# Optimization experiments

Measured on AMD Instinct MI355X. Metric: run time of the kernel, lower is better.

The kernel has to match this reference:

```python
import jax, jax.numpy as jnp
import numpy as np

B, D, C = 2048, 512, 50000
MARGIN = 0.3
SCALE = 30.0
EPS = 1e-12


def setup_inputs() -> dict:
    key = jax.random.key(0)
    k1, k2, k3 = jax.random.split(key, 3)
    embeddings = jax.random.normal(k1, (B, D), dtype=jnp.float32)
    labels = jax.random.randint(k2, (B,), 0, C, dtype=jnp.int64)
    # Xavier-uniform init for weight (num_classes, in_features)
    limit = float(np.sqrt(6.0 / (C + D)))
    weight = jax.random.uniform(k3, (C, D), dtype=jnp.float32, minval=-limit, maxval=limit)
    return {"embeddings": embeddings, "labels": labels, "weight": weight}


def _l2_normalize(x, axis):
    # Matches torch F.normalize(p=2, eps=1e-12): x / max(||x||, eps)
    norm = jnp.sqrt(jnp.sum(x * x, axis=axis, keepdims=True))
    return x / jnp.maximum(norm, EPS)


def reference(embeddings, labels, weight):
    emb_n = _l2_normalize(embeddings, axis=1)            # (B, D)
    w_n = _l2_normalize(weight, axis=1)                  # (C, D)
    cos = jnp.einsum("bd,cd->bc", emb_n, w_n)            # (B, C)
    # margin subtract at label index (avoid dense one-hot materialization)
    rows = jnp.arange(cos.shape[0])
    phi = cos.at[rows, labels].add(-MARGIN)
    logits = phi * SCALE
    # cross-entropy with mean reduction
    logp = jax.nn.log_softmax(logits, axis=-1)
    nll = -jnp.take_along_axis(logp, labels[:, None], axis=-1)[:, 0]
    return jnp.mean(nll)
```

## Files before the change

kernel.cpp:

```cpp
#include <hip/hip_runtime.h>
#include <hip/hip_bf16.h>
#include <math.h>
#include <stdint.h>


#define B_ROWS    2048
#define D_DIM     512
#define C_CLASSES 50000
#define C_PAD     50048
#define NCHUNK    391
#define CPX       49
#define ARC_MARGIN 0.3f
#define ARC_SCALE  30.0f
#define ARC_EPS    1e-12f
#define K_LOG2E_S  43.2808512f

#define OFF_WQ    0u
#define OFF_EMBQ  25624576u
#define OFF_WINV  26673152u
#define OFF_EINV  26873152u
#define OFF_PART  26881344u

typedef __attribute__((ext_vector_type(8))) int   i32x8;
typedef __attribute__((ext_vector_type(4))) int   i32x4;
typedef __attribute__((ext_vector_type(4))) float f32x4;

typedef __attribute__((address_space(1))) const unsigned int g_u32;
typedef __attribute__((address_space(3))) unsigned int       l_u32;

__device__ __forceinline__ void gload_lds16(const void* g, void* l) {
    g_u32* gp = (g_u32*)(uintptr_t)g;
    l_u32* lp = (l_u32*)(uintptr_t)l;
    __builtin_amdgcn_global_load_lds(gp, lp, 16, 0, 0);
}

__global__ __launch_bounds__(256) void k_prep(const float* __restrict__ emb,
                                              const float* __restrict__ weight,
                                              uint8_t* __restrict__ embq,
                                              uint8_t* __restrict__ wq,
                                              float* __restrict__ einv,
                                              float* __restrict__ winv,
                                              float* __restrict__ out) {
    if (blockIdx.x == 0 && threadIdx.x == 0) out[0] = 0.f;
    int gw   = (blockIdx.x * blockDim.x + threadIdx.x) >> 6;
    int lane = threadIdx.x & 63;
    const float* src;
    uint8_t* dst;
    float* invout;
    if (gw < C_PAD) {
        if (gw >= C_CLASSES) {
            *(int2*)(wq + (size_t)gw * D_DIM + lane * 8) = make_int2(0, 0);
            return;
        }
        src = weight + (size_t)gw * D_DIM;
        dst = wq + (size_t)gw * D_DIM;
        invout = winv + gw;
    } else {
        int row = gw - C_PAD;
        src = emb + (size_t)row * D_DIM;
        dst = embq + (size_t)row * D_DIM;
        invout = einv + row;
    }
    const float4* r4 = (const float4*)src;
    float4 v0 = r4[lane * 2];
    float4 v1 = r4[lane * 2 + 1];
    float s = v0.x*v0.x + v0.y*v0.y + v0.z*v0.z + v0.w*v0.w
            + v1.x*v1.x + v1.y*v1.y + v1.z*v1.z + v1.w*v1.w;
    #pragma unroll
    for (int off = 32; off; off >>= 1) s += __shfl_xor(s, off);
    float r = 1.0f / fmaxf(sqrtf(s), ARC_EPS);
    if (lane == 0) *invout = r;
    int p0 = __builtin_amdgcn_cvt_pk_fp8_f32(v0.x * r, v0.y * r, 0, false);
    p0     = __builtin_amdgcn_cvt_pk_fp8_f32(v0.z * r, v0.w * r, p0, true);
    int p1 = __builtin_amdgcn_cvt_pk_fp8_f32(v1.x * r, v1.y * r, 0, false);
    p1     = __builtin_amdgcn_cvt_pk_fp8_f32(v1.z * r, v1.w * r, p1, true);
    *(int2*)(dst + lane * 8) = make_int2(p0, p1);
}

struct TrueT  { static constexpr bool value = true;  };
struct FalseT { static constexpr bool value = false; };

__global__ __launch_bounds__(256) void k_gemm(const uint8_t* __restrict__ embq,
                                              const uint8_t* __restrict__ wq,
                                              float* __restrict__ partials) {
    __shared__ __align__(16) uint8_t A_s[128 * 128];
    __shared__ __align__(16) uint8_t B_s[128 * 128];
    __shared__ float Red[128][2];

    const int tid    = threadIdx.x;
    const int w      = tid >> 6;
    const int lane   = tid & 63;
    const int lanelo = lane & 15;
    const int quad   = lane >> 4;
    const int wrow0  = (w >> 1) * 64;
    const int wcol0  = (w & 1) * 64;

    const int id    = blockIdx.x;
    const int xcd   = id & 7;
    const int s     = id >> 3;
    const int rb_   = s & 15;
    const int chunk = xcd * CPX + (s >> 4);
    if (chunk >= NCHUNK) return;
    const int b0 = rb_ * 128;
    const int n0 = chunk * 128;

    const uint8_t* Abase = embq + (size_t)b0 * D_DIM;
    const uint8_t* Bbase = wq   + (size_t)n0 * D_DIM;

    f32x4 acc[4][4];
    #pragma unroll
    for (int i = 0; i < 4; ++i)
        #pragma unroll
        for (int j = 0; j < 4; ++j)
            acc[i][j] = (f32x4){0.f, 0.f, 0.f, 0.f};

    const int srow = lane & 15;
    const int skc  = lane >> 4;

    auto stage = [&](int kt) {
        const int k0 = kt * 128;
        #pragma unroll
        for (int t = 0; t < 2; ++t) {
            const int rb = w * 2 + t;
            #pragma unroll
            for (int h = 0; h < 2; ++h) {
                const int kc = h * 4 + skc;
                gload_lds16(Abase + (size_t)(rb * 16 + srow) * D_DIM + k0 + kc * 16,
                            &A_s[rb * 2048 + h * 1024]);
                gload_lds16(Bbase + (size_t)(rb * 16 + srow) * D_DIM + k0 + kc * 16,
                            &B_s[rb * 2048 + h * 1024]);
            }
        }
    };

    stage(0);
    #pragma unroll
    for (int kt = 0; kt < 4; ++kt) {
        __syncthreads();

        i32x8 af[4], bfr[4];
        #pragma unroll
        for (int i = 0; i < 4; ++i) {
            const int rb = (w >> 1) * 4 + i;
            i32x4 lo = *(const i32x4*)&A_s[rb * 2048 + quad * 512 + lanelo * 16];
            i32x4 hi = *(const i32x4*)&A_s[rb * 2048 + quad * 512 + 256 + lanelo * 16];
            af[i] = (i32x8){lo[0], lo[1], lo[2], lo[3], hi[0], hi[1], hi[2], hi[3]};
        }
        #pragma unroll
        for (int j = 0; j < 4; ++j) {
            const int rb = (w & 1) * 4 + j;
            i32x4 lo = *(const i32x4*)&B_s[rb * 2048 + quad * 512 + lanelo * 16];
            i32x4 hi = *(const i32x4*)&B_s[rb * 2048 + quad * 512 + 256 + lanelo * 16];
            bfr[j] = (i32x8){lo[0], lo[1], lo[2], lo[3], hi[0], hi[1], hi[2], hi[3]};
        }
        __syncthreads();

        if (kt < 3) stage(kt + 1);

        #pragma unroll
        for (int i = 0; i < 4; ++i)
            #pragma unroll
            for (int j = 0; j < 4; ++j)
                acc[i][j] = __builtin_amdgcn_mfma_scale_f32_16x16x128_f8f6f4(
                    af[i], bfr[j], acc[i][j],
                    0, 0,
                    0, 127,
                    0, 127);
    }

    auto epi = [&](auto maskTag) {
        constexpr bool MASK = decltype(maskTag)::value;
        #pragma unroll
        for (int i = 0; i < 4; ++i) {
            #pragma unroll
            for (int reg = 0; reg < 4; ++reg) {
                float s4 = 0.f;
                #pragma unroll
                for (int j = 0; j < 4; ++j) {
                    float t = __builtin_amdgcn_exp2f(
                        fmaf(acc[i][j][reg], K_LOG2E_S, -K_LOG2E_S));
                    if (MASK) {
                        int c = n0 + wcol0 + j * 16 + lanelo;
                        if (c >= C_CLASSES) t = 0.f;
                    }
                    s4 += t;
                }
                #pragma unroll
                for (int off = 1; off < 16; off <<= 1)
                    s4 += __shfl_xor(s4, off);
                if (lanelo == 0)
                    Red[wrow0 + i * 16 + quad * 4 + reg][w & 1] = s4;
            }
        }
    };
    if (chunk == NCHUNK - 1) epi(TrueT{}); else epi(FalseT{});
    __syncthreads();

    if (tid < 128)
        partials[(size_t)(b0 + tid) * NCHUNK + chunk] = Red[tid][0] + Red[tid][1];
}

__global__ __launch_bounds__(256) void k_fin(const float* __restrict__ emb,
                                             const float* __restrict__ weight,
                                             const float* __restrict__ einv,
                                             const float* __restrict__ winv,
                                             const int* __restrict__ labels,
                                             const float* __restrict__ partials,
                                             float* __restrict__ out) {
    __shared__ float sm[4];
    int widx = threadIdx.x >> 6;
    int b    = blockIdx.x * 4 + widx;
    int lane = threadIdx.x & 63;
    int label = labels[b];

    const float4* e  = (const float4*)(emb + (size_t)b * D_DIM);
    const float4* wt = (const float4*)(weight + (size_t)label * D_DIM);
    float4 e0 = e[lane],  e1 = e[lane + 64];
    float4 w0 = wt[lane], w1 = wt[lane + 64];
    float dot = e0.x*w0.x + e0.y*w0.y + e0.z*w0.z + e0.w*w0.w
              + e1.x*w1.x + e1.y*w1.y + e1.z*w1.z + e1.w*w1.w;
    float ls = 0.f;
    for (int idx = lane; idx < NCHUNK; idx += 64)
        ls += partials[(size_t)b * NCHUNK + idx];
    #pragma unroll
    for (int off = 32; off; off >>= 1) {
        dot += __shfl_xor(dot, off);
        ls  += __shfl_xor(ls, off);
    }

    float cosv   = dot * einv[b] * winv[label];
    float l_orig = ARC_SCALE * cosv;
    float l_adj  = ARC_SCALE * (cosv - ARC_MARGIN);

    float s_adj = ls - __expf(l_orig - ARC_SCALE) + __expf(l_adj - ARC_SCALE);
    float v = ARC_SCALE + logf(s_adj) - l_adj;
    if (lane == 0) sm[widx] = v;
    __syncthreads();
    if (threadIdx.x == 0)
        atomicAdd(out, (sm[0] + sm[1] + sm[2] + sm[3]) * (1.0f / (float)B_ROWS));
}

extern "C" void kernel_launch(void* const* d_in, const int* in_sizes, int n_in,
                              void* d_out, int out_size, void* d_ws, size_t ws_size,
                              hipStream_t stream) {
    const float* emb    = (const float*)d_in[0];
    const int*   labels = (const int*)d_in[1];
    const float* weight = (const float*)d_in[2];
    float* out = (float*)d_out;

    char* ws = (char*)d_ws;
    uint8_t* wq    = (uint8_t*)(ws + OFF_WQ);
    uint8_t* embq  = (uint8_t*)(ws + OFF_EMBQ);
    float* winv     = (float*)(ws + OFF_WINV);
    float* einv     = (float*)(ws + OFF_EINV);
    float* partials = (float*)(ws + OFF_PART);

    k_prep<<<(C_PAD + B_ROWS) / 4, 256, 0, stream>>>(emb, weight, embq, wq,
                                                     einv, winv, out);

    k_gemm<<<8 * CPX * 16, 256, 0, stream>>>(embq, wq, partials);

    k_fin<<<B_ROWS / 4, 256, 0, stream>>>(emb, weight, einv, winv, labels,
                                          partials, out);
}
```

Measured before the change: 268.1 us.

## Load A fragments from global, double-buffer B in LDS, transpose-reduce epilogue

The A (embedding) tile is no longer staged in LDS; each wave reads its MFMA A fragments straight from global memory. The freed LDS holds a double buffer for the B (weight) tile, so the next k-step prefetch is issued right after a single barrier, and the second barrier per iteration is removed. The epilogue swaps 16 separate 4-step shuffle reductions for a butterfly transpose-reduce that needs 15 shuffles total, and launch bounds ask for 4 blocks per CU. The cost is redundant, uncoalesced global reads of A across the waves and blocks that share a row block, plus possible register pressure from the occupancy hint.

```diff
diff --git a/kernel.cpp b/kernel.cpp
--- a/kernel.cpp
+++ b/kernel.cpp
@@ -80,11 +80,10 @@
 struct TrueT  { static constexpr bool value = true;  };
 struct FalseT { static constexpr bool value = false; };
 
-__global__ __launch_bounds__(256) void k_gemm(const uint8_t* __restrict__ embq,
-                                              const uint8_t* __restrict__ wq,
-                                              float* __restrict__ partials) {
-    __shared__ __align__(16) uint8_t A_s[128 * 128];
-    __shared__ __align__(16) uint8_t B_s[128 * 128];
+__global__ __launch_bounds__(256, 4) void k_gemm(const uint8_t* __restrict__ embq,
+                                                 const uint8_t* __restrict__ wq,
+                                                 float* __restrict__ partials) {
+    __shared__ __align__(16) uint8_t B_s[2][16384];
     __shared__ float Red[128][2];
 
     const int tid    = threadIdx.x;
@@ -97,9 +96,9 @@
 
     const int id    = blockIdx.x;
     const int xcd   = id & 7;
-    const int s     = id >> 3;
-    const int rb_   = s & 15;
-    const int chunk = xcd * CPX + (s >> 4);
+    const int s_    = id >> 3;
+    const int rb_   = s_ & 15;
+    const int chunk = xcd * CPX + (s_ >> 4);
     if (chunk >= NCHUNK) return;
     const int b0 = rb_ * 128;
     const int n0 = chunk * 128;
@@ -117,7 +116,7 @@
     const int srow = lane & 15;
     const int skc  = lane >> 4;
 
-    auto stage = [&](int kt) {
+    auto stageB = [&](int kt, uint8_t* dst) {
         const int k0 = kt * 128;
         #pragma unroll
         for (int t = 0; t < 2; ++t) {
@@ -125,50 +124,54 @@
             #pragma unroll
             for (int h = 0; h < 2; ++h) {
                 const int kc = h * 4 + skc;
-                gload_lds16(Abase + (size_t)(rb * 16 + srow) * D_DIM + k0 + kc * 16,
-                            &A_s[rb * 2048 + h * 1024]);
                 gload_lds16(Bbase + (size_t)(rb * 16 + srow) * D_DIM + k0 + kc * 16,
-                            &B_s[rb * 2048 + h * 1024]);
+                            dst + rb * 2048 + h * 1024);
             }
         }
     };
 
-    stage(0);
+    auto loadA = [&](int i, int kt) -> i32x8 {
+        const uint8_t* p = Abase
+            + (size_t)(((w >> 1) * 4 + i) * 16 + lanelo) * D_DIM
+            + kt * 128 + quad * 32;
+        i32x4 lo = *(const i32x4*)p;
+        i32x4 hi = *(const i32x4*)(p + 16);
+        return (i32x8){lo[0], lo[1], lo[2], lo[3], hi[0], hi[1], hi[2], hi[3]};
+    };
+
+    stageB(0, B_s[0]);
     #pragma unroll
     for (int kt = 0; kt < 4; ++kt) {
+        uint8_t* cur = B_s[kt & 1];
         __syncthreads();
-
-        i32x8 af[4], bfr[4];
-        #pragma unroll
-        for (int i = 0; i < 4; ++i) {
-            const int rb = (w >> 1) * 4 + i;
-            i32x4 lo = *(const i32x4*)&A_s[rb * 2048 + quad * 512 + lanelo * 16];
-            i32x4 hi = *(const i32x4*)&A_s[rb * 2048 + quad * 512 + 256 + lanelo * 16];
-            af[i] = (i32x8){lo[0], lo[1], lo[2], lo[3], hi[0], hi[1], hi[2], hi[3]};
-        }
+        if (kt < 3) stageB(kt + 1, B_s[(kt & 1) ^ 1]);
+
+        i32x8 bfr[4];
         #pragma unroll
         for (int j = 0; j < 4; ++j) {
             const int rb = (w & 1) * 4 + j;
-            i32x4 lo = *(const i32x4*)&B_s[rb * 2048 + quad * 512 + lanelo * 16];
-            i32x4 hi = *(const i32x4*)&B_s[rb * 2048 + quad * 512 + 256 + lanelo * 16];
+            i32x4 lo = *(const i32x4*)&cur[rb * 2048 + quad * 512 + lanelo * 16];
+            i32x4 hi = *(const i32x4*)&cur[rb * 2048 + quad * 512 + 256 + lanelo * 16];
             bfr[j] = (i32x8){lo[0], lo[1], lo[2], lo[3], hi[0], hi[1], hi[2], hi[3]};
         }
-        __syncthreads();
-
-        if (kt < 3) stage(kt + 1);
-
-        #pragma unroll
-        for (int i = 0; i < 4; ++i)
+
+        #pragma unroll
+        for (int ip = 0; ip < 4; ip += 2) {
+            i32x8 a0 = loadA(ip, kt);
+            i32x8 a1 = loadA(ip + 1, kt);
             #pragma unroll
             for (int j = 0; j < 4; ++j)
-                acc[i][j] = __builtin_amdgcn_mfma_scale_f32_16x16x128_f8f6f4(
-                    af[i], bfr[j], acc[i][j],
-                    0, 0,
-                    0, 127,
-                    0, 127);
-    }
-
-    auto epi = [&](auto maskTag) {
+                acc[ip][j] = __builtin_amdgcn_mfma_scale_f32_16x16x128_f8f6f4(
+                    a0, bfr[j], acc[ip][j], 0, 0, 0, 127, 0, 127);
+            #pragma unroll
+            for (int j = 0; j < 4; ++j)
+                acc[ip + 1][j] = __builtin_amdgcn_mfma_scale_f32_16x16x128_f8f6f4(
+                    a1, bfr[j], acc[ip + 1][j], 0, 0, 0, 127, 0, 127);
+        }
+    }
+
+    float s[16];
+    auto fill = [&](auto maskTag) {
         constexpr bool MASK = decltype(maskTag)::value;
         #pragma unroll
         for (int i = 0; i < 4; ++i) {
@@ -185,15 +188,27 @@
                     }
                     s4 += t;
                 }
-                #pragma unroll
-                for (int off = 1; off < 16; off <<= 1)
-                    s4 += __shfl_xor(s4, off);
-                if (lanelo == 0)
-                    Red[wrow0 + i * 16 + quad * 4 + reg][w & 1] = s4;
+                s[i * 4 + reg] = s4;
             }
         }
     };
-    if (chunk == NCHUNK - 1) epi(TrueT{}); else epi(FalseT{});
+    if (chunk == NCHUNK - 1) fill(TrueT{}); else fill(FalseT{});
+
+    #pragma unroll
+    for (int m = 8; m >= 1; m >>= 1) {
+        bool upper = (lanelo & m) != 0;
+        #pragma unroll
+        for (int t = 0; t < m; ++t) {
+            float lo = s[t], hi = s[t + m];
+            float send = upper ? lo : hi;
+            float recv = __shfl_xor(send, m);
+            s[t] = (upper ? hi : lo) + recv;
+        }
+    }
+    {
+        int row = wrow0 + (lanelo >> 2) * 16 + quad * 4 + (lanelo & 3);
+        Red[row][w & 1] = s[0];
+    }
     __syncthreads();
 
     if (tid < 128)
```

Measured after the change: 306.5 us. 14.3% more time.
